# Performance work log

Measured on AMD Instinct MI355X. Metric: run time of the kernel, lower is better.

The kernel has to match this reference:

```python
import jax, jax.numpy as jnp
import numpy as np

K = 9          # number of umbrella neighbors (excluding self)
BN_EPS = 1e-5


def setup_inputs() -> dict:
    key = jax.random.key(0)
    ks = jax.random.split(key, 8)
    B, N, C = 4, 8192, 3
    ch = 7
    x = jax.random.normal(ks[0], (B, N, C), jnp.float32)
    w1 = jax.random.normal(ks[1], (ch, ch), jnp.float32) * 0.4
    gamma1 = jnp.ones((ch,), jnp.float32)
    beta1 = jnp.zeros((ch,), jnp.float32)
    w2 = jax.random.normal(ks[2], (ch, ch), jnp.float32) * 0.4
    bias2 = jax.random.normal(ks[3], (ch,), jnp.float32) * 0.1
    gamma2 = jnp.ones((ch,), jnp.float32)
    beta2 = jnp.zeros((ch,), jnp.float32)
    w3 = jax.random.normal(ks[4], (ch, ch), jnp.float32) * 0.4
    bias3 = jax.random.normal(ks[5], (ch,), jnp.float32) * 0.1
    return dict(x=x, w1=w1, gamma1=gamma1, beta1=beta1, w2=w2, bias2=bias2,
                gamma2=gamma2, beta2=beta2, w3=w3, bias3=bias3)


def _bn(t, gamma, beta):
    # BatchNorm2d in training mode: batch stats over (B, N, K) per channel (last dim)
    m = t.mean(axis=(0, 1, 2))
    v = t.var(axis=(0, 1, 2))  # biased, matching torch BN normalization
    return (t - m) * jax.lax.rsqrt(v + BN_EPS) * gamma + beta


def reference(x, w1, gamma1, beta1, w2, bias2, gamma2, beta2, w3, bias3):
    B, N, _ = x.shape
    # ---- kNN (negative squared distance, top-k largest == nearest) ----
    xsq = jnp.sum(x * x, axis=-1)                       # [B,N]
    xx = jnp.einsum('bnc,bmc->bnm', x, x)               # [B,N,N]
    dist = 2.0 * xx - xsq[:, :, None] - xsq[:, None, :]
    idx = jax.lax.top_k(dist, K + 1)[1]                 # [B,N,K+1], includes self
    # ---- gather neighbor coords, recenter, drop self ----
    nbr = jax.vmap(lambda xb, ib: xb[ib])(x, idx)       # [B,N,K+1,3]
    nbr = nbr - x[:, :, None, :]
    nbr = nbr[:, :, 1:, :]                              # [B,N,K,3]
    # ---- sort neighbors by azimuth phi ----
    phi = jnp.arctan2(nbr[..., 1], nbr[..., 0]) / (2.0 * np.pi) + 0.5
    order = jnp.argsort(phi, axis=-1)                   # [B,N,K]
    srt = jnp.take_along_axis(nbr, order[..., None], axis=2)  # [B,N,K,3]
    # ---- umbrella pairs: (v_i, v_{i+1 mod K}) ----
    v1 = srt
    v2 = jnp.roll(srt, -1, axis=2)
    centroids = 0.5 * (v1 + v2)                         # [B,N,K,3]
    normals = jnp.cross(v1, v2) + 1e-5
    normals = normals / jnp.linalg.norm(normals, axis=-1, keepdims=True)
    # flip so the first normal's x-component is positive (per point)
    pos_mask = (normals[:, :, 0:1, 0] > 0).astype(x.dtype) * 2.0 - 1.0  # [B,N,1]
    normals = normals * pos_mask[..., None]
    positions = jnp.sum(centroids * normals, axis=-1) / jnp.sqrt(jnp.asarray(3.0, x.dtype))
    feat = jnp.concatenate([centroids, normals, positions[..., None]], axis=-1)  # [B,N,K,7]
    # ---- tiny 1x1 conv MLP (channel-last einsum) + BN + ReLU ----
    h = jnp.einsum('bnkc,oc->bnko', feat, w1)
    h = jax.nn.relu(_bn(h, gamma1, beta1))
    h = jnp.einsum('bnkc,oc->bnko', h, w2) + bias2
    h = jax.nn.relu(_bn(h, gamma2, beta2))
    h = jnp.einsum('bnkc,oc->bnko', h, w3) + bias3
    pooled = jnp.max(h, axis=2)                         # [B,N,7]
    return jnp.concatenate([x, pooled], axis=-1)        # [B,N,10]
```

## Files before the change

### kernel.cpp

```cpp
#include <hip/hip_runtime.h>
#include <math.h>

#define BB 4
#define NN 8192
#define TOTAL (BB*NN)
#define KNBR 9
#define CH 7
#define NCHUNK 16
#define CHUNK (NN/NCHUNK)
#define SLOTS 8
#define NROWS (NCHUNK*SLOTS/2)
#define QB 4
#define BN_EPS 1e-5f
#define M_ELEMS (TOTAL*KNBR)
#define NREP 16

#define OFF_PTS   0
#define OFF_PI    524288
#define OFF_STATS 8912896
#define OFF_H1    8914944
#define OFF_H2    0

__device__ __forceinline__ void ibody(float (&dl)[10], int (&il)[10], float d, int ii) {
    bool c0 = d > dl[0];
#pragma unroll
    for (int p = 9; p > 0; p--) {
        bool here = d > dl[p];
        bool up   = d > dl[p-1];
        float nd = up ? dl[p-1] : d;
        int   ni = up ? il[p-1] : ii;
        if (here) { dl[p] = nd; il[p] = ni; }
    }
    if (c0) { dl[0] = d; il[0] = ii; }
}

__device__ __forceinline__ void insert10(float (&dl)[10], int (&il)[10], float d, int ii) {
    if (d > dl[9]) ibody(dl, il, d, ii);
}

__global__ __launch_bounds__(256) void knn_k(const float* __restrict__ x,
                                             float4* __restrict__ pts,
                                             unsigned int* __restrict__ pi,
                                             float* __restrict__ stats) {
    const int b = blockIdx.z, chunk = blockIdx.y;
    const int c0 = chunk * CHUNK;

    if (blockIdx.x == 0 && blockIdx.y == 0 && blockIdx.z == 0) {
        for (int i = threadIdx.x; i < NREP*28; i += 256) stats[i] = 0.f;
    }

    __shared__ float4 tile[CHUNK];
    if (threadIdx.x < CHUNK/4) {
        const float4* __restrict__ x4 = (const float4*)(x + (long)(b*NN + c0)*3);
        int t = threadIdx.x;
        float4 f0 = x4[3*t], f1 = x4[3*t+1], f2 = x4[3*t+2];
        float px[4] = {f0.x, f0.w, f1.z, f2.y};
        float py[4] = {f0.y, f1.x, f1.w, f2.z};
        float pz[4] = {f0.z, f1.y, f2.x, f2.w};
#pragma unroll
        for (int u = 0; u < 4; u++) {
            float sq = __fadd_rn(__fadd_rn(__fmul_rn(px[u],px[u]), __fmul_rn(py[u],py[u])),
                                 __fmul_rn(pz[u],pz[u]));
            tile[4*t+u] = make_float4(px[u], py[u], pz[u], sq);
        }
    }
    __syncthreads();

    if (blockIdx.x == 0) {
#pragma unroll
        for (int j = 0; j < CHUNK/256; j++)
            pts[b*NN + c0 + threadIdx.x + j*256] = tile[threadIdx.x + j*256];
    }

    const int q0 = blockIdx.x * (256*QB) + threadIdx.x;
    float qx2[QB], qy2[QB], qz2[QB], nqb[QB];
#pragma unroll
    for (int v = 0; v < QB; v++) {
        long qoff = (long)(b*NN + q0 + v*256) * 3;
        float qx = x[qoff], qy = x[qoff+1], qz = x[qoff+2];
        float qw = qx*qx + qy*qy + qz*qz;
        qx2[v] = qx + qx; qy2[v] = qy + qy; qz2[v] = qz + qz;
        nqb[v] = -1.0f - qw;
    }

    unsigned int m[QB][SLOTS];
#pragma unroll
    for (int v = 0; v < QB; v++)
#pragma unroll
        for (int s = 0; s < SLOTS; s++) m[v][s] = 0xFFFFFFFFu;

#pragma unroll 4
    for (int j = 0; j < CHUNK; j++) {
        float4 t = tile[j];
#pragma unroll
        for (int v = 0; v < QB; v++) {
            float d = fmaf(qx2[v], t.x, fmaf(qy2[v], t.y, fmaf(qz2[v], t.z, nqb[v] - t.w)));
            unsigned int kd = (__float_as_uint(d) & 0xFFFFFE00u) | (unsigned int)j;
#pragma unroll
            for (int p = SLOTS-1; p >= 1; p--)
                asm("v_med3_u32 %0, %1, %2, %3" : "=v"(m[v][p]) : "v"(kd), "v"(m[v][p-1]), "v"(m[v][p]));
            m[v][0] = kd < m[v][0] ? kd : m[v][0];
        }
    }

#pragma unroll
    for (int v = 0; v < QB; v++) {
        int idx[SLOTS];
#pragma unroll
        for (int s = 0; s < SLOTS; s++) idx[s] = (int)(m[v][s] & 511u);
#pragma unroll
        for (int r = 0; r < SLOTS; r++) {
#pragma unroll
            for (int i = (r & 1); i + 1 < SLOTS; i += 2) {
                int a = idx[i], c = idx[i+1];
                idx[i] = min(a, c); idx[i+1] = max(a, c);
            }
        }
        int g = b*NN + q0 + v*256;
#pragma unroll
        for (int s2 = 0; s2 < SLOTS/2; s2++) {
            unsigned int lo = (unsigned int)(c0 + idx[2*s2]);
            unsigned int hi = (unsigned int)(c0 + idx[2*s2+1]);
            pi[(long)(chunk*(SLOTS/2) + s2)*TOTAL + g] = lo | (hi << 16);
        }
    }
}

__global__ __launch_bounds__(128) void geom_k(const float4* __restrict__ pts,
                                              const unsigned int* __restrict__ pi,
                                              const float* __restrict__ w1,
                                              float* __restrict__ h1, float* __restrict__ stats) {
    __shared__ float sw1[49];
    __shared__ float acc[14];
    if (threadIdx.x < 49) sw1[threadIdx.x] = w1[threadIdx.x];
    if (threadIdx.x < 14) acc[threadIdx.x] = 0.f;
    __syncthreads();

    int g = blockIdx.x * 128 + threadIdx.x;
    int b = g >> 13, n = g & (NN-1);
    const float4* __restrict__ base = pts + b*NN;
    float4 qp = base[n];
    float qn = -qp.w;

    float dl[10]; int il[10];
#pragma unroll
    for (int j = 0; j < 10; j++) { dl[j] = -INFINITY; il[j] = 0; }
#pragma unroll
    for (int h = 0; h < 2; h++) {
        unsigned int pk[32];
#pragma unroll
        for (int u = 0; u < 32; u++) pk[u] = pi[(long)(h*32 + u)*TOTAL + g];
#pragma unroll
        for (int bt = 0; bt < 4; bt++) {
            int id[16];
#pragma unroll
            for (int u = 0; u < 8; u++) {
                id[2*u]   = (int)(pk[bt*8 + u] & 0xFFFFu);
                id[2*u+1] = (int)(pk[bt*8 + u] >> 16);
            }
            float4 pp[16];
#pragma unroll
            for (int v = 0; v < 16; v++) pp[v] = base[id[v]];
            float dd[16];
#pragma unroll
            for (int v = 0; v < 16; v++) {
                float dot2 = __fadd_rn(__fadd_rn(__fmul_rn(qp.x, 2.f*pp[v].x),
                                                 __fmul_rn(qp.y, 2.f*pp[v].y)),
                                       __fmul_rn(qp.z, 2.f*pp[v].z));
                dd[v] = __fsub_rn(__fadd_rn(dot2, qn), pp[v].w);
            }
#pragma unroll
            for (int v = 0; v < 16; v++) insert10(dl, il, dd[v], id[v]);
        }
    }

    float vx[9], vy[9], vz[9], ph[9];
#pragma unroll
    for (int t = 0; t < 9; t++) {
        float4 p4 = base[il[t+1]];
        vx[t] = p4.x - qp.x; vy[t] = p4.y - qp.y; vz[t] = p4.z - qp.z;
        ph[t] = atan2f(vy[t], vx[t]) / 6.283185307179586f + 0.5f;
    }

    int rank[9];
#pragma unroll
    for (int t = 0; t < 9; t++) {
        int r = 0;
#pragma unroll
        for (int u = 0; u < 9; u++) {
            if (u == t) continue;
            bool before = (ph[u] < ph[t]) || (ph[u] == ph[t] && u < t);
            r += before ? 1 : 0;
        }
        rank[t] = r;
    }
    float sx[9], sy[9], sz[9];
#pragma unroll
    for (int s = 0; s < 9; s++) {
        float a = 0.f, bb = 0.f, c = 0.f;
#pragma unroll
        for (int t = 0; t < 9; t++) {
            bool m = (rank[t] == s);
            a = m ? vx[t] : a; bb = m ? vy[t] : bb; c = m ? vz[t] : c;
        }
        sx[s] = a; sy[s] = bb; sz[s] = c;
    }

    float sgn;
    {
        float ax = sx[0], ay = sy[0], az = sz[0];
        float bx = sx[1], by = sy[1], bz = sz[1];
        float nx0 = ay*bz - az*by + 1e-5f;
        float ny0 = az*bx - ax*bz + 1e-5f;
        float nz0 = ax*by - ay*bx + 1e-5f;
        float inv = 1.0f / sqrtf(nx0*nx0 + ny0*ny0 + nz0*nz0);
        sgn = (nx0*inv > 0.0f) ? 1.0f : -1.0f;
    }

    float sum[7], sumsq[7];
#pragma unroll
    for (int o = 0; o < 7; o++) { sum[o] = 0.f; sumsq[o] = 0.f; }

#pragma unroll
    for (int t = 0; t < 9; t++) {
        const int t2 = (t + 1) % 9;
        float ax = sx[t],  ay = sy[t],  az = sz[t];
        float bx = sx[t2], by = sy[t2], bz = sz[t2];
        float cx = 0.5f*(ax+bx), cy = 0.5f*(ay+by), cz = 0.5f*(az+bz);
        float nx0 = ay*bz - az*by + 1e-5f;
        float ny0 = az*bx - ax*bz + 1e-5f;
        float nz0 = ax*by - ay*bx + 1e-5f;
        float inv = 1.0f / sqrtf(nx0*nx0 + ny0*ny0 + nz0*nz0);
        float nx = nx0*inv*sgn, ny = ny0*inv*sgn, nz = nz0*inv*sgn;
        float pos = (cx*nx + cy*ny + cz*nz) / 1.7320508075688772f;

        float f[7] = {cx, cy, cz, nx, ny, nz, pos};
        float* outp = h1 + ((long)g*9 + t) * 7;
#pragma unroll
        for (int o = 0; o < 7; o++) {
            float h = 0.f;
#pragma unroll
            for (int c = 0; c < 7; c++) h += f[c] * sw1[o*7 + c];
            outp[o] = h;
            sum[o] += h; sumsq[o] += h*h;
        }
    }

#pragma unroll
    for (int o = 0; o < 7; o++) {
        float s  = sum[o];
        float s2 = sumsq[o];
        for (int off = 32; off > 0; off >>= 1) { s += __shfl_down(s, off); s2 += __shfl_down(s2, off); }
        if ((threadIdx.x & 63) == 0) {
            atomicAdd(&acc[o], s);
            atomicAdd(&acc[7 + o], s2);
        }
    }
    __syncthreads();
    if (threadIdx.x < 14)
        atomicAdd(&stats[(blockIdx.x & (NREP-1))*28 + threadIdx.x], acc[threadIdx.x]);
}

__global__ __launch_bounds__(256) void mm2_k(const float* __restrict__ h1,
                                             const float* __restrict__ gamma1, const float* __restrict__ beta1,
                                             const float* __restrict__ w2, const float* __restrict__ bias2,
                                             float* __restrict__ h2, float* __restrict__ stats) {
    int g = blockIdx.x * 256 + threadIdx.x;
    const float invM = 1.0f / (float)M_ELEMS;
    float s1[7], b1[7];
#pragma unroll
    for (int c = 0; c < 7; c++) {
        float sm = 0.f, sq = 0.f;
#pragma unroll
        for (int r = 0; r < NREP; r++) { sm += stats[r*28 + c]; sq += stats[r*28 + 7 + c]; }
        float m = sm * invM;
        float v = sq * invM - m*m;
        float sc = gamma1[c] / sqrtf(v + BN_EPS);
        s1[c] = sc; b1[c] = beta1[c] - m*sc;
    }
    float a[7];
    const float* hh = h1 + (long)g * 7;
#pragma unroll
    for (int c = 0; c < 7; c++) a[c] = fmaxf(hh[c]*s1[c] + b1[c], 0.0f);

    float sum[7], sumsq[7];
#pragma unroll
    for (int o = 0; o < 7; o++) {
        float h = 0.f;
#pragma unroll
        for (int c = 0; c < 7; c++) h += a[c] * w2[o*7 + c];
        h += bias2[o];
        h2[(long)g*7 + o] = h;
        sum[o] = h; sumsq[o] = h*h;
    }

    __shared__ float acc[14];
    if (threadIdx.x < 14) acc[threadIdx.x] = 0.f;
    __syncthreads();
#pragma unroll
    for (int o = 0; o < 7; o++) {
        float s  = sum[o];
        float s2 = sumsq[o];
        for (int off = 32; off > 0; off >>= 1) { s += __shfl_down(s, off); s2 += __shfl_down(s2, off); }
        if ((threadIdx.x & 63) == 0) {
            atomicAdd(&acc[o], s);
            atomicAdd(&acc[7 + o], s2);
        }
    }
    __syncthreads();
    if (threadIdx.x < 14)
        atomicAdd(&stats[(blockIdx.x & (NREP-1))*28 + 14 + threadIdx.x], acc[threadIdx.x]);
}

__global__ __launch_bounds__(128) void final_k(const float* __restrict__ x,
                                               const float* __restrict__ h2,
                                               const float* __restrict__ gamma2, const float* __restrict__ beta2,
                                               const float* __restrict__ w3, const float* __restrict__ bias3,
                                               const float* __restrict__ stats, float* __restrict__ out) {
    int g = blockIdx.x * 128 + threadIdx.x;
    const float invM = 1.0f / (float)M_ELEMS;
    float s2v[7], b2v[7];
#pragma unroll
    for (int c = 0; c < 7; c++) {
        float sm = 0.f, sq = 0.f;
#pragma unroll
        for (int r = 0; r < NREP; r++) { sm += stats[r*28 + 14 + c]; sq += stats[r*28 + 21 + c]; }
        float m = sm * invM;
        float v = sq * invM - m*m;
        float sc = gamma2[c] / sqrtf(v + BN_EPS);
        s2v[c] = sc; b2v[c] = beta2[c] - m*sc;
    }
    float pooled[7];
#pragma unroll
    for (int o = 0; o < 7; o++) pooled[o] = -INFINITY;

    const float* hh = h2 + (long)g * 63;
#pragma unroll
    for (int t = 0; t < 9; t++) {
        float a[7];
#pragma unroll
        for (int c = 0; c < 7; c++) a[c] = fmaxf(hh[t*7 + c]*s2v[c] + b2v[c], 0.0f);
#pragma unroll
        for (int o = 0; o < 7; o++) {
            float h = 0.f;
#pragma unroll
            for (int c = 0; c < 7; c++) h += a[c] * w3[o*7 + c];
            h += bias3[o];
            pooled[o] = fmaxf(pooled[o], h);
        }
    }
    out[g*10 + 0] = x[g*3 + 0];
    out[g*10 + 1] = x[g*3 + 1];
    out[g*10 + 2] = x[g*3 + 2];
#pragma unroll
    for (int o = 0; o < 7; o++) out[g*10 + 3 + o] = pooled[o];
}

extern "C" void kernel_launch(void* const* d_in, const int* in_sizes, int n_in,
                              void* d_out, int out_size, void* d_ws, size_t ws_size,
                              hipStream_t stream) {
    const float* x      = (const float*)d_in[0];
    const float* w1     = (const float*)d_in[1];
    const float* gamma1 = (const float*)d_in[2];
    const float* beta1  = (const float*)d_in[3];
    const float* w2     = (const float*)d_in[4];
    const float* bias2  = (const float*)d_in[5];
    const float* gamma2 = (const float*)d_in[6];
    const float* beta2  = (const float*)d_in[7];
    const float* w3     = (const float*)d_in[8];
    const float* bias3  = (const float*)d_in[9];
    float* out = (float*)d_out;

    char* ws = (char*)d_ws;
    float4*       pts  = (float4*)(ws + OFF_PTS);
    unsigned int* pi   = (unsigned int*)(ws + OFF_PI);
    float*        h1   = (float*)(ws + OFF_H1);
    float*        h2   = (float*)(ws + OFF_H2);
    float*        stats= (float*)(ws + OFF_STATS);

    knn_k  <<<dim3(NN/(256*QB), NCHUNK, BB), 256, 0, stream>>>(x, pts, pi, stats);
    geom_k <<<TOTAL/128, 128, 0, stream>>>(pts, pi, w1, h1, stats);
    mm2_k  <<<M_ELEMS/256, 256, 0, stream>>>(h1, gamma1, beta1, w2, bias2, h2, stats);
    final_k<<<TOTAL/128, 128, 0, stream>>>(x, h2, gamma2, beta2, w3, bias3, stats, out);
}
```

Before: 228.7 us.

## Fuse geometry, BN and MLP stages into one persistent kernel with grid barriers

Merges geom_k, mm2_k and final_k into a single kernel of 256 blocks that keeps each point's 63 intermediate activations in registers. The two BatchNorm statistic reductions are separated by software grid barriers built on atomic counters. This removes the global-memory round trips for h1 and h2 and two kernel launches. In exchange it relies on all 256 blocks being co-resident, adds spin-wait barrier latency, and raises register pressure from the 63-float array.

New measurement: 244.6 us. 6.9% more time.

```diff
diff --git a/kernel.cpp b/kernel.cpp
--- a/kernel.cpp
+++ b/kernel.cpp
@@ -14,12 +14,11 @@
 #define BN_EPS 1e-5f
 #define M_ELEMS (TOTAL*KNBR)
 #define NREP 16
+#define NBLK 256
 
 #define OFF_PTS   0
 #define OFF_PI    524288
 #define OFF_STATS 8912896
-#define OFF_H1    8914944
-#define OFF_H2    0
 
 __device__ __forceinline__ void ibody(float (&dl)[10], int (&il)[10], float d, int ii) {
     bool c0 = d > dl[0];
@@ -46,7 +45,7 @@
     const int c0 = chunk * CHUNK;
 
     if (blockIdx.x == 0 && blockIdx.y == 0 && blockIdx.z == 0) {
-        for (int i = threadIdx.x; i < NREP*28; i += 256) stats[i] = 0.f;
+        for (int i = threadIdx.x; i < NREP*28 + 8; i += 256) stats[i] = 0.f;
     }
 
     __shared__ float4 tile[CHUNK];
@@ -126,16 +125,39 @@
     }
 }
 
-__global__ __launch_bounds__(128) void geom_k(const float4* __restrict__ pts,
-                                              const unsigned int* __restrict__ pi,
-                                              const float* __restrict__ w1,
-                                              float* __restrict__ h1, float* __restrict__ stats) {
-    __shared__ float sw1[49];
+__device__ __forceinline__ void grid_barrier(int* cnt) {
+    __syncthreads();
+    if (threadIdx.x == 0) {
+        __threadfence();
+        __hip_atomic_fetch_add(cnt, 1, __ATOMIC_RELEASE, __HIP_MEMORY_SCOPE_AGENT);
+        while (__hip_atomic_load(cnt, __ATOMIC_ACQUIRE, __HIP_MEMORY_SCOPE_AGENT) < NBLK)
+            __builtin_amdgcn_s_sleep(8);
+    }
+    __syncthreads();
+}
+
+__global__ __launch_bounds__(128, 1) void fused_k(const float* __restrict__ x,
+                                                  const float4* __restrict__ pts,
+                                                  const unsigned int* __restrict__ pi,
+                                                  const float* __restrict__ w1,
+                                                  const float* __restrict__ gamma1, const float* __restrict__ beta1,
+                                                  const float* __restrict__ w2, const float* __restrict__ bias2,
+                                                  const float* __restrict__ gamma2, const float* __restrict__ beta2,
+                                                  const float* __restrict__ w3, const float* __restrict__ bias3,
+                                                  float* __restrict__ stats, float* __restrict__ out) {
+    __shared__ float sw1[49], sw2[49], sw3[49], sb2[7], sb3[7];
     __shared__ float acc[14];
-    if (threadIdx.x < 49) sw1[threadIdx.x] = w1[threadIdx.x];
+    __shared__ float sco[14];
+    if (threadIdx.x < 49) {
+        sw1[threadIdx.x] = w1[threadIdx.x];
+        sw2[threadIdx.x] = w2[threadIdx.x];
+        sw3[threadIdx.x] = w3[threadIdx.x];
+    }
+    if (threadIdx.x < 7) { sb2[threadIdx.x] = bias2[threadIdx.x]; sb3[threadIdx.x] = bias3[threadIdx.x]; }
     if (threadIdx.x < 14) acc[threadIdx.x] = 0.f;
     __syncthreads();
 
+    int* cnt = (int*)(stats + NREP*28);
     int g = blockIdx.x * 128 + threadIdx.x;
     int b = g >> 13, n = g & (NN-1);
     const float4* __restrict__ base = pts + b*NN;
@@ -217,6 +239,7 @@
         sgn = (nx0*inv > 0.0f) ? 1.0f : -1.0f;
     }
 
+    float hv[63];
     float sum[7], sumsq[7];
 #pragma unroll
     for (int o = 0; o < 7; o++) { sum[o] = 0.f; sumsq[o] = 0.f; }
@@ -235,13 +258,12 @@
         float pos = (cx*nx + cy*ny + cz*nz) / 1.7320508075688772f;
 
         float f[7] = {cx, cy, cz, nx, ny, nz, pos};
-        float* outp = h1 + ((long)g*9 + t) * 7;
 #pragma unroll
         for (int o = 0; o < 7; o++) {
             float h = 0.f;
 #pragma unroll
             for (int c = 0; c < 7; c++) h += f[c] * sw1[o*7 + c];
-            outp[o] = h;
+            hv[t*7 + o] = h;
             sum[o] += h; sumsq[o] += h*h;
         }
     }
@@ -259,44 +281,43 @@
     __syncthreads();
     if (threadIdx.x < 14)
         atomicAdd(&stats[(blockIdx.x & (NREP-1))*28 + threadIdx.x], acc[threadIdx.x]);
-}
-
-__global__ __launch_bounds__(256) void mm2_k(const float* __restrict__ h1,
-                                             const float* __restrict__ gamma1, const float* __restrict__ beta1,
-                                             const float* __restrict__ w2, const float* __restrict__ bias2,
-                                             float* __restrict__ h2, float* __restrict__ stats) {
-    int g = blockIdx.x * 256 + threadIdx.x;
+
+    grid_barrier(&cnt[0]);
+
     const float invM = 1.0f / (float)M_ELEMS;
-    float s1[7], b1[7];
-#pragma unroll
-    for (int c = 0; c < 7; c++) {
+    if (threadIdx.x < 7) {
+        int c = threadIdx.x;
         float sm = 0.f, sq = 0.f;
 #pragma unroll
-        for (int r = 0; r < NREP; r++) { sm += stats[r*28 + c]; sq += stats[r*28 + 7 + c]; }
+        for (int r = 0; r < NREP; r++) {
+            sm += __hip_atomic_load(&stats[r*28 + c],     __ATOMIC_RELAXED, __HIP_MEMORY_SCOPE_AGENT);
+            sq += __hip_atomic_load(&stats[r*28 + 7 + c], __ATOMIC_RELAXED, __HIP_MEMORY_SCOPE_AGENT);
+        }
         float m = sm * invM;
         float v = sq * invM - m*m;
         float sc = gamma1[c] / sqrtf(v + BN_EPS);
-        s1[c] = sc; b1[c] = beta1[c] - m*sc;
-    }
-    float a[7];
-    const float* hh = h1 + (long)g * 7;
-#pragma unroll
-    for (int c = 0; c < 7; c++) a[c] = fmaxf(hh[c]*s1[c] + b1[c], 0.0f);
-
-    float sum[7], sumsq[7];
-#pragma unroll
-    for (int o = 0; o < 7; o++) {
-        float h = 0.f;
-#pragma unroll
-        for (int c = 0; c < 7; c++) h += a[c] * w2[o*7 + c];
-        h += bias2[o];
-        h2[(long)g*7 + o] = h;
-        sum[o] = h; sumsq[o] = h*h;
-    }
-
-    __shared__ float acc[14];
-    if (threadIdx.x < 14) acc[threadIdx.x] = 0.f;
-    __syncthreads();
+        sco[c] = sc; sco[7 + c] = beta1[c] - m*sc;
+    }
+    if (threadIdx.x >= 64 && threadIdx.x < 78) acc[threadIdx.x - 64] = 0.f;
+    __syncthreads();
+
+#pragma unroll
+    for (int o = 0; o < 7; o++) { sum[o] = 0.f; sumsq[o] = 0.f; }
+#pragma unroll
+    for (int t = 0; t < 9; t++) {
+        float a[7];
+#pragma unroll
+        for (int c = 0; c < 7; c++) a[c] = fmaxf(hv[t*7 + c]*sco[c] + sco[7 + c], 0.0f);
+#pragma unroll
+        for (int o = 0; o < 7; o++) {
+            float h = 0.f;
+#pragma unroll
+            for (int c = 0; c < 7; c++) h += a[c] * sw2[o*7 + c];
+            h += sb2[o];
+            hv[t*7 + o] = h;
+            sum[o] += h; sumsq[o] += h*h;
+        }
+    }
 #pragma unroll
     for (int o = 0; o < 7; o++) {
         float s  = sum[o];
@@ -310,48 +331,44 @@
     __syncthreads();
     if (threadIdx.x < 14)
         atomicAdd(&stats[(blockIdx.x & (NREP-1))*28 + 14 + threadIdx.x], acc[threadIdx.x]);
-}
-
-__global__ __launch_bounds__(128) void final_k(const float* __restrict__ x,
-                                               const float* __restrict__ h2,
-                                               const float* __restrict__ gamma2, const float* __restrict__ beta2,
-                                               const float* __restrict__ w3, const float* __restrict__ bias3,
-                                               const float* __restrict__ stats, float* __restrict__ out) {
-    int g = blockIdx.x * 128 + threadIdx.x;
-    const float invM = 1.0f / (float)M_ELEMS;
-    float s2v[7], b2v[7];
-#pragma unroll
-    for (int c = 0; c < 7; c++) {
+
+    grid_barrier(&cnt[1]);
+
+    if (threadIdx.x < 7) {
+        int c = threadIdx.x;
         float sm = 0.f, sq = 0.f;
 #pragma unroll
-        for (int r = 0; r < NREP; r++) { sm += stats[r*28 + 14 + c]; sq += stats[r*28 + 21 + c]; }
+        for (int r = 0; r < NREP; r++) {
+            sm += __hip_atomic_load(&stats[r*28 + 14 + c], __ATOMIC_RELAXED, __HIP_MEMORY_SCOPE_AGENT);
+            sq += __hip_atomic_load(&stats[r*28 + 21 + c], __ATOMIC_RELAXED, __HIP_MEMORY_SCOPE_AGENT);
+        }
         float m = sm * invM;
         float v = sq * invM - m*m;
         float sc = gamma2[c] / sqrtf(v + BN_EPS);
-        s2v[c] = sc; b2v[c] = beta2[c] - m*sc;
-    }
+        sco[c] = sc; sco[7 + c] = beta2[c] - m*sc;
+    }
+    __syncthreads();
+
     float pooled[7];
 #pragma unroll
     for (int o = 0; o < 7; o++) pooled[o] = -INFINITY;
-
-    const float* hh = h2 + (long)g * 63;
 #pragma unroll
     for (int t = 0; t < 9; t++) {
         float a[7];
 #pragma unroll
-        for (int c = 0; c < 7; c++) a[c] = fmaxf(hh[t*7 + c]*s2v[c] + b2v[c], 0.0f);
+        for (int c = 0; c < 7; c++) a[c] = fmaxf(hv[t*7 + c]*sco[c] + sco[7 + c], 0.0f);
 #pragma unroll
         for (int o = 0; o < 7; o++) {
             float h = 0.f;
 #pragma unroll
-            for (int c = 0; c < 7; c++) h += a[c] * w3[o*7 + c];
-            h += bias3[o];
+            for (int c = 0; c < 7; c++) h += a[c] * sw3[o*7 + c];
+            h += sb3[o];
             pooled[o] = fmaxf(pooled[o], h);
         }
     }
-    out[g*10 + 0] = x[g*3 + 0];
-    out[g*10 + 1] = x[g*3 + 1];
-    out[g*10 + 2] = x[g*3 + 2];
+    out[g*10 + 0] = qp.x;
+    out[g*10 + 1] = qp.y;
+    out[g*10 + 2] = qp.z;
 #pragma unroll
     for (int o = 0; o < 7; o++) out[g*10 + 3 + o] = pooled[o];
 }
@@ -374,12 +391,9 @@
     char* ws = (char*)d_ws;
     float4*       pts  = (float4*)(ws + OFF_PTS);
     unsigned int* pi   = (unsigned int*)(ws + OFF_PI);
-    float*        h1   = (float*)(ws + OFF_H1);
-    float*        h2   = (float*)(ws + OFF_H2);
     float*        stats= (float*)(ws + OFF_STATS);
 
     knn_k  <<<dim3(NN/(256*QB), NCHUNK, BB), 256, 0, stream>>>(x, pts, pi, stats);
-    geom_k <<<TOTAL/128, 128, 0, stream>>>(pts, pi, w1, h1, stats);
-    mm2_k  <<<M_ELEMS/256, 256, 0, stream>>>(h1, gamma1, beta1, w2, bias2, h2, stats);
-    final_k<<<TOTAL/128, 128, 0, stream>>>(x, h2, gamma2, beta2, w3, bias3, stats, out);
-}
+    fused_k<<<NBLK, 128, 0, stream>>>(x, pts, pi, w1, gamma1, beta1, w2, bias2,
+                                      gamma2, beta2, w3, bias3, stats, out);
+}
```

## Recompute second MLP layer in final kernel and retile kNN to 8 queries per thread

Applied to the files above, without the earlier changes.

The second conv layer output is no longer written to global memory. The stats pass now only accumulates BN2 statistics, and the final kernel recomputes layer 2 from h1 before applying BN2, layer 3 and the max-pool. This removes one full write and one read of the 7-channel intermediate, at the cost of duplicating the small 7x7 matmul. Separately, the kNN kernel moves to 128-thread blocks with 8 queries per thread and a lower unroll, raising register reuse of each tile load but also register pressure.

Result: slower. 342.5 us (+49.7%).

```diff
diff --git a/kernel.cpp b/kernel.cpp
--- a/kernel.cpp
+++ b/kernel.cpp
@@ -10,7 +10,8 @@
 #define CHUNK (NN/NCHUNK)
 #define SLOTS 8
 #define NROWS (NCHUNK*SLOTS/2)
-#define QB 4
+#define QB 8
+#define KT 128
 #define BN_EPS 1e-5f
 #define M_ELEMS (TOTAL*KNBR)
 #define NREP 16
@@ -19,7 +20,6 @@
 #define OFF_PI    524288
 #define OFF_STATS 8912896
 #define OFF_H1    8914944
-#define OFF_H2    0
 
 __device__ __forceinline__ void ibody(float (&dl)[10], int (&il)[10], float d, int ii) {
     bool c0 = d > dl[0];
@@ -38,19 +38,19 @@
     if (d > dl[9]) ibody(dl, il, d, ii);
 }
 
-__global__ __launch_bounds__(256) void knn_k(const float* __restrict__ x,
-                                             float4* __restrict__ pts,
-                                             unsigned int* __restrict__ pi,
-                                             float* __restrict__ stats) {
+__global__ __launch_bounds__(KT) void knn_k(const float* __restrict__ x,
+                                            float4* __restrict__ pts,
+                                            unsigned int* __restrict__ pi,
+                                            float* __restrict__ stats) {
     const int b = blockIdx.z, chunk = blockIdx.y;
     const int c0 = chunk * CHUNK;
 
     if (blockIdx.x == 0 && blockIdx.y == 0 && blockIdx.z == 0) {
-        for (int i = threadIdx.x; i < NREP*28; i += 256) stats[i] = 0.f;
+        for (int i = threadIdx.x; i < NREP*28; i += KT) stats[i] = 0.f;
     }
 
     __shared__ float4 tile[CHUNK];
-    if (threadIdx.x < CHUNK/4) {
+    {
         const float4* __restrict__ x4 = (const float4*)(x + (long)(b*NN + c0)*3);
         int t = threadIdx.x;
         float4 f0 = x4[3*t], f1 = x4[3*t+1], f2 = x4[3*t+2];
@@ -68,15 +68,15 @@
 
     if (blockIdx.x == 0) {
 #pragma unroll
-        for (int j = 0; j < CHUNK/256; j++)
-            pts[b*NN + c0 + threadIdx.x + j*256] = tile[threadIdx.x + j*256];
-    }
-
-    const int q0 = blockIdx.x * (256*QB) + threadIdx.x;
+        for (int j = 0; j < CHUNK/KT; j++)
+            pts[b*NN + c0 + threadIdx.x + j*KT] = tile[threadIdx.x + j*KT];
+    }
+
+    const int q0 = blockIdx.x * (KT*QB) + threadIdx.x;
     float qx2[QB], qy2[QB], qz2[QB], nqb[QB];
 #pragma unroll
     for (int v = 0; v < QB; v++) {
-        long qoff = (long)(b*NN + q0 + v*256) * 3;
+        long qoff = (long)(b*NN + q0 + v*KT) * 3;
         float qx = x[qoff], qy = x[qoff+1], qz = x[qoff+2];
         float qw = qx*qx + qy*qy + qz*qz;
         qx2[v] = qx + qx; qy2[v] = qy + qy; qz2[v] = qz + qz;
@@ -89,7 +89,7 @@
 #pragma unroll
         for (int s = 0; s < SLOTS; s++) m[v][s] = 0xFFFFFFFFu;
 
-#pragma unroll 4
+#pragma unroll 2
     for (int j = 0; j < CHUNK; j++) {
         float4 t = tile[j];
 #pragma unroll
@@ -116,7 +116,7 @@
                 idx[i] = min(a, c); idx[i+1] = max(a, c);
             }
         }
-        int g = b*NN + q0 + v*256;
+        int g = b*NN + q0 + v*KT;
 #pragma unroll
         for (int s2 = 0; s2 < SLOTS/2; s2++) {
             unsigned int lo = (unsigned int)(c0 + idx[2*s2]);
@@ -261,10 +261,10 @@
         atomicAdd(&stats[(blockIdx.x & (NREP-1))*28 + threadIdx.x], acc[threadIdx.x]);
 }
 
-__global__ __launch_bounds__(256) void mm2_k(const float* __restrict__ h1,
-                                             const float* __restrict__ gamma1, const float* __restrict__ beta1,
-                                             const float* __restrict__ w2, const float* __restrict__ bias2,
-                                             float* __restrict__ h2, float* __restrict__ stats) {
+__global__ __launch_bounds__(256) void stats2_k(const float* __restrict__ h1,
+                                                const float* __restrict__ gamma1, const float* __restrict__ beta1,
+                                                const float* __restrict__ w2, const float* __restrict__ bias2,
+                                                float* __restrict__ stats) {
     int g = blockIdx.x * 256 + threadIdx.x;
     const float invM = 1.0f / (float)M_ELEMS;
     float s1[7], b1[7];
@@ -290,7 +290,6 @@
 #pragma unroll
         for (int c = 0; c < 7; c++) h += a[c] * w2[o*7 + c];
         h += bias2[o];
-        h2[(long)g*7 + o] = h;
         sum[o] = h; sumsq[o] = h*h;
     }
 
@@ -313,38 +312,58 @@
 }
 
 __global__ __launch_bounds__(128) void final_k(const float* __restrict__ x,
-                                               const float* __restrict__ h2,
+                                               const float* __restrict__ h1,
+                                               const float* __restrict__ gamma1, const float* __restrict__ beta1,
+                                               const float* __restrict__ w2, const float* __restrict__ bias2,
                                                const float* __restrict__ gamma2, const float* __restrict__ beta2,
                                                const float* __restrict__ w3, const float* __restrict__ bias3,
                                                const float* __restrict__ stats, float* __restrict__ out) {
     int g = blockIdx.x * 128 + threadIdx.x;
     const float invM = 1.0f / (float)M_ELEMS;
-    float s2v[7], b2v[7];
+    float s1v[7], b1v[7], s2v[7], b2v[7];
 #pragma unroll
     for (int c = 0; c < 7; c++) {
-        float sm = 0.f, sq = 0.f;
-#pragma unroll
-        for (int r = 0; r < NREP; r++) { sm += stats[r*28 + 14 + c]; sq += stats[r*28 + 21 + c]; }
-        float m = sm * invM;
-        float v = sq * invM - m*m;
-        float sc = gamma2[c] / sqrtf(v + BN_EPS);
-        s2v[c] = sc; b2v[c] = beta2[c] - m*sc;
+        float sm1 = 0.f, sq1 = 0.f, sm2 = 0.f, sq2 = 0.f;
+#pragma unroll
+        for (int r = 0; r < NREP; r++) {
+            sm1 += stats[r*28 + c];      sq1 += stats[r*28 + 7 + c];
+            sm2 += stats[r*28 + 14 + c]; sq2 += stats[r*28 + 21 + c];
+        }
+        float m1 = sm1 * invM;
+        float v1 = sq1 * invM - m1*m1;
+        float sc1 = gamma1[c] / sqrtf(v1 + BN_EPS);
+        s1v[c] = sc1; b1v[c] = beta1[c] - m1*sc1;
+        float m2 = sm2 * invM;
+        float v2 = sq2 * invM - m2*m2;
+        float sc2 = gamma2[c] / sqrtf(v2 + BN_EPS);
+        s2v[c] = sc2; b2v[c] = beta2[c] - m2*sc2;
     }
     float pooled[7];
 #pragma unroll
     for (int o = 0; o < 7; o++) pooled[o] = -INFINITY;
 
-    const float* hh = h2 + (long)g * 63;
+    const float* hh = h1 + (long)g * 63;
 #pragma unroll
     for (int t = 0; t < 9; t++) {
         float a[7];
 #pragma unroll
-        for (int c = 0; c < 7; c++) a[c] = fmaxf(hh[t*7 + c]*s2v[c] + b2v[c], 0.0f);
+        for (int c = 0; c < 7; c++) a[c] = fmaxf(hh[t*7 + c]*s1v[c] + b1v[c], 0.0f);
+        float h2r[7];
 #pragma unroll
         for (int o = 0; o < 7; o++) {
             float h = 0.f;
 #pragma unroll
-            for (int c = 0; c < 7; c++) h += a[c] * w3[o*7 + c];
+            for (int c = 0; c < 7; c++) h += a[c] * w2[o*7 + c];
+            h2r[o] = h + bias2[o];
+        }
+        float a2[7];
+#pragma unroll
+        for (int c = 0; c < 7; c++) a2[c] = fmaxf(h2r[c]*s2v[c] + b2v[c], 0.0f);
+#pragma unroll
+        for (int o = 0; o < 7; o++) {
+            float h = 0.f;
+#pragma unroll
+            for (int c = 0; c < 7; c++) h += a2[c] * w3[o*7 + c];
             h += bias3[o];
             pooled[o] = fmaxf(pooled[o], h);
         }
@@ -374,12 +393,12 @@
     char* ws = (char*)d_ws;
     float4*       pts  = (float4*)(ws + OFF_PTS);
     unsigned int* pi   = (unsigned int*)(ws + OFF_PI);
+    float*        stats= (float*)(ws + OFF_STATS);
     float*        h1   = (float*)(ws + OFF_H1);
-    float*        h2   = (float*)(ws + OFF_H2);
-    float*        stats= (float*)(ws + OFF_STATS);
-
-    knn_k  <<<dim3(NN/(256*QB), NCHUNK, BB), 256, 0, stream>>>(x, pts, pi, stats);
-    geom_k <<<TOTAL/128, 128, 0, stream>>>(pts, pi, w1, h1, stats);
-    mm2_k  <<<M_ELEMS/256, 256, 0, stream>>>(h1, gamma1, beta1, w2, bias2, h2, stats);
-    final_k<<<TOTAL/128, 128, 0, stream>>>(x, h2, gamma2, beta2, w3, bias3, stats, out);
-}
+
+    knn_k   <<<dim3(NN/(KT*QB), NCHUNK, BB), KT, 0, stream>>>(x, pts, pi, stats);
+    geom_k  <<<TOTAL/128, 128, 0, stream>>>(pts, pi, w1, h1, stats);
+    stats2_k<<<M_ELEMS/256, 256, 0, stream>>>(h1, gamma1, beta1, w2, bias2, stats);
+    final_k <<<TOTAL/128, 128, 0, stream>>>(x, h1, gamma1, beta1, w2, bias2,
+                                            gamma2, beta2, w3, bias3, stats, out);
+}
```
